# Kernel tuning notes

Hardware: AMD Instinct MI355X
Metric: run time of the kernel (lower is better)

The kernel has to match this reference:

```python
import jax, jax.numpy as jnp
import numpy as np

NUM_HEAD = 8
D_K = 64


def setup_inputs() -> dict:
    key = jax.random.key(0)
    k1, k2, k3 = jax.random.split(key, 3)
    B, S, D = 8, 1024, 512
    input_x = jax.random.normal(k1, (B, S, D), dtype=jnp.float32)
    W_qkv = jax.random.normal(k2, (D, 3 * D), dtype=jnp.float32) * 0.02
    W_out = jax.random.normal(k3, (D, D), dtype=jnp.float32) * 0.02
    return {"input_x": input_x, "W_qkv": W_qkv, "W_out": W_out}


def reference(input_x, W_qkv, W_out):
    B, S, D = input_x.shape
    H, dk = NUM_HEAD, D_K
    qkv = input_x @ W_qkv  # (B, S, 3*D)
    # Faithful to the source: per-head slices OVERLAP.
    # head h: Q=qkv[h*dk:(h+1)*dk], K=qkv[(h+1)*dk:(h+2)*dk], V=qkv[(h+2)*dk:(h+3)*dk]
    Q = qkv[:, :, 0:H * dk].reshape(B, S, H, dk)
    K = qkv[:, :, dk:dk + H * dk].reshape(B, S, H, dk)
    V = qkv[:, :, 2 * dk:2 * dk + H * dk].reshape(B, S, H, dk)
    scale = jnp.asarray(1.0 / np.sqrt(dk), dtype=qkv.dtype)
    scores = jnp.einsum('bqhd,bkhd->bhqk', Q, K) * scale  # (B, H, S, S)
    # nn.Softmax() with dim=None on a 3D (B,S,S) tensor -> legacy dim=0 (batch axis)
    attn = jax.nn.softmax(scores, axis=0)
    out = jnp.einsum('bhqk,bkhd->bqhd', attn, V).reshape(B, S, H * dk)
    return out @ W_out
```

## Files before the change

kernel.cpp:

```cpp
#include <hip/hip_runtime.h>

typedef __bf16 bf16x8 __attribute__((ext_vector_type(8)));
typedef float  f32x4  __attribute__((ext_vector_type(4)));
typedef unsigned short u16x8 __attribute__((ext_vector_type(8)));
typedef unsigned short USHORT;
typedef unsigned int   u32;

__device__ __forceinline__ USHORT f2bf(float f) {
    unsigned u = __float_as_uint(f);
    u += 0x7fffu + ((u >> 16) & 1u);
    return (USHORT)(u >> 16);
}

__device__ __forceinline__ float bf2f(USHORT v) {
    return __uint_as_float((unsigned)v << 16);
}

__device__ __forceinline__ u32 packbf(float lo, float hi) {
    return (u32)f2bf(lo) | ((u32)f2bf(hi) << 16);
}

__device__ __forceinline__ f32x4 fz4() { f32x4 z = {0.f, 0.f, 0.f, 0.f}; return z; }

__device__ __forceinline__ bf16x8 ldbf8(const USHORT* p) { return *(const bf16x8*)p; }

__device__ __forceinline__ f32x4 mfma16(bf16x8 a, bf16x8 b, f32x4 c) {
    return __builtin_amdgcn_mfma_f32_16x16x32_bf16(a, b, c, 0, 0, 0);
}

__device__ __forceinline__ void gload_lds16(const void* g, void* s) {
    __builtin_amdgcn_global_load_lds(
        (const __attribute__((address_space(1))) unsigned int*)g,
        (__attribute__((address_space(3))) unsigned int*)s, 16, 0, 0);
}

__device__ __forceinline__ void lds_fence() {
    asm volatile("s_waitcnt lgkmcnt(0)" ::: "memory");
    __builtin_amdgcn_sched_barrier(0);
}

__global__ __launch_bounds__(256) void prep_kernel(const float* __restrict__ X,
                                                   const float* __restrict__ Wqkv,
                                                   const float* __restrict__ Wout,
                                                   USHORT* __restrict__ Xb,
                                                   USHORT* __restrict__ Wt1,
                                                   USHORT* __restrict__ Wt3) {
    int bid = blockIdx.x;
    if (bid < 2048) {
        int base = (bid * 256 + threadIdx.x) * 8;
        float4 a = *(const float4*)(X + base);
        float4 b = *(const float4*)(X + base + 4);
        u16x8 o;
        o[0] = f2bf(a.x); o[1] = f2bf(a.y); o[2] = f2bf(a.z); o[3] = f2bf(a.w);
        o[4] = f2bf(b.x); o[5] = f2bf(b.y); o[6] = f2bf(b.z); o[7] = f2bf(b.w);
        *(u16x8*)(Xb + base) = o;
    } else if (bid < 3328) {
        int t = (bid - 2048) * 256 + threadIdx.x;
        int k = t & 511, n = t >> 9;
        Wt1[t] = f2bf(Wqkv[(size_t)k * 1536 + n]);
    } else {
        int t = (bid - 3328) * 256 + threadIdx.x;
        int k = t & 511, n = t >> 9;
        Wt3[t] = f2bf(Wout[(size_t)k * 512 + n]);
    }
}

__global__ __launch_bounds__(256) void reduce2(const USHORT* __restrict__ a,
                                               const USHORT* __restrict__ b,
                                               USHORT* __restrict__ o) {
    int base = (blockIdx.x * 256 + threadIdx.x) * 8;
    u16x8 va = *(const u16x8*)(a + base);
    u16x8 vb = *(const u16x8*)(b + base);
    u16x8 out;
#pragma unroll
    for (int j = 0; j < 8; ++j)
        out[j] = f2bf(bf2f(va[j]) + bf2f(vb[j]));
    *(u16x8*)(o + base) = out;
}

template <bool BF16OUT>
__global__ __launch_bounds__(256) void gemm_bt(const USHORT* __restrict__ A,
                                               const USHORT* __restrict__ Bt,
                                               void* __restrict__ Cv,
                                               int M, int N, int K) {
    __shared__ __align__(16) USHORT Asm[128 * 32];
    __shared__ __align__(16) USHORT Bsm[128 * 32];
    const int tid = threadIdx.x;
    const int wv = tid >> 6, ln = tid & 63;
    const int l16 = ln & 15, quad = ln >> 4;
    const int m0 = blockIdx.x * 128, n0 = blockIdx.y * 128;
    const int wm = (wv >> 1) * 64, wn = (wv & 1) * 64;

    f32x4 acc[4][4];
#pragma unroll
    for (int i = 0; i < 4; ++i)
#pragma unroll
        for (int j = 0; j < 4; ++j) acc[i][j] = fz4();

    const int kTiles = K >> 5;
    for (int kt = 0; kt < kTiles; ++kt) {
        __syncthreads();
#pragma unroll
        for (int i = 0; i < 2; ++i) {
            int cb = wv * 128 + i * 64;
            int c = cb + ln;
            gload_lds16(A + (size_t)(m0 + (c >> 2)) * K + kt * 32 + (c & 3) * 8,
                        &Asm[cb * 8]);
            gload_lds16(Bt + (size_t)(n0 + (c >> 2)) * K + kt * 32 + (c & 3) * 8,
                        &Bsm[cb * 8]);
        }
        __syncthreads();

        bf16x8 af[4], bfr[4];
#pragma unroll
        for (int i = 0; i < 4; ++i)
            af[i] = ldbf8(&Asm[(wm + i * 16 + l16) * 32 + quad * 8]);
#pragma unroll
        for (int j = 0; j < 4; ++j)
            bfr[j] = ldbf8(&Bsm[(wn + j * 16 + l16) * 32 + quad * 8]);
#pragma unroll
        for (int i = 0; i < 4; ++i)
#pragma unroll
            for (int j = 0; j < 4; ++j)
                acc[i][j] = mfma16(af[i], bfr[j], acc[i][j]);
    }

#pragma unroll
    for (int i = 0; i < 4; ++i)
#pragma unroll
        for (int j = 0; j < 4; ++j)
#pragma unroll
            for (int r = 0; r < 4; ++r) {
                size_t row = m0 + wm + i * 16 + quad * 4 + r;
                size_t col = n0 + wn + j * 16 + l16;
                if (BF16OUT)
                    ((USHORT*)Cv)[row * N + col] = f2bf(acc[i][j][r]);
                else
                    ((float*)Cv)[row * N + col] = acc[i][j][r];
            }
}

__global__ __launch_bounds__(256) void transpose_v(const USHORT* __restrict__ P,
                                                   USHORT* __restrict__ Vt) {
    __shared__ __align__(16) USHORT T[64][72];
    const int t = threadIdx.x;
    const int k0 = blockIdx.x * 64;
    const int hh = blockIdx.y;
    const int b = blockIdx.z;
#pragma unroll
    for (int i = 0; i < 2; ++i) {
        int c = i * 256 + t;
        int kk = c >> 3, d8 = (c & 7) * 8;
        u16x8 v = *(const u16x8*)(P + (size_t)((b << 10) + k0 + kk) * 640 +
                                  (hh + 2) * 64 + d8);
        *(u16x8*)&T[kk][d8] = v;
    }
    __syncthreads();
#pragma unroll
    for (int i = 0; i < 2; ++i) {
        int d = (t >> 3) + i * 32;
        int kk0 = (t & 7) * 8;
        u16x8 v;
#pragma unroll
        for (int j = 0; j < 8; ++j) v[j] = T[kk0 + j][d];
        *(u16x8*)(Vt + (size_t)(((b << 3) + hh) * 64 + d) * 1024 + k0 + kk0) = v;
    }
}

__global__ __launch_bounds__(256, 1) void attn_kernel(const USHORT* __restrict__ P,
                                                      const USHORT* __restrict__ Vt,
                                                      USHORT* __restrict__ pt0,
                                                      USHORT* __restrict__ pt1) {
    const int bid = blockIdx.x;
    const int g = bid & 15;
    const int h = g >> 1;
    const int kc = g & 1;
    const int qb = bid >> 4;
    const int tid = threadIdx.x;
    const int wv = tid >> 6;
    const int lane = tid & 63;
    const int l16 = lane & 15, quad = lane >> 4;
    const int q0 = qb * 64 + wv * 16;

    __shared__ __align__(16) USHORT Kl[2][16384];
    __shared__ __align__(16) USHORT Vl[2][16384];

    const int qhalf = quad >> 1;
    const bool qodd = (quad & 1) != 0;
    const bool qhi  = quad >= 2;
    const int idx01 = ((qodd ? (2 + qhalf) : qhalf) * 16 + l16) * 4;
    const int idx23 = ((qodd ? qhalf : (2 + qhalf)) * 16 + l16) * 4;

    bf16x8 qf[8][2];
#pragma unroll
    for (int b = 0; b < 8; ++b)
#pragma unroll
        for (int ks = 0; ks < 2; ++ks)
            qf[b][ks] = ldbf8(P + (size_t)((b << 10) + q0 + l16) * 640 + h * 64 +
                              ks * 32 + quad * 8);

    f32x4 oacc[8][4];
#pragma unroll
    for (int b = 0; b < 8; ++b)
#pragma unroll
        for (int nt = 0; nt < 4; ++nt) oacc[b][nt] = fz4();

    auto stage = [&](int k0s, int buf) {
        if (wv < 2) {
#pragma unroll
            for (int i = 0; i < 16; ++i) {
                int gg = wv * 16 + i;
                int b = gg >> 2, ks = (gg >> 1) & 1, half = gg & 1;
                gload_lds16(P + (size_t)((b << 10) + k0s + half * 16 + (lane & 15)) * 640 +
                                (h + 1) * 64 + ks * 32 + (lane >> 4) * 8,
                            &Kl[buf][(b * 2 + ks) * 1024 + half * 512]);
            }
        } else {
#pragma unroll
            for (int i = 0; i < 16; ++i) {
                int gg = (wv - 2) * 16 + i;
                int b = gg >> 2, dq = gg & 3;
                gload_lds16(Vt + (size_t)(((b << 3) + h) * 64 + dq * 16 + (lane & 15)) * 1024 +
                                k0s + (lane >> 4) * 8,
                            &Vl[buf][b * 2048 + dq * 512]);
            }
        }
    };

    const int kbase = kc * 512;
    stage(kbase, 0);
    __syncthreads();

    int buf = 0;
    for (int it = 0; it < 16; ++it) {
        if (it < 15) stage(kbase + (it + 1) * 32, buf ^ 1);

        const USHORT* Kb = Kl[buf];
        const USHORT* Vb = Vl[buf];

        f32x4 sacc[8][2];
#pragma unroll
        for (int b = 0; b < 8; ++b) { sacc[b][0] = fz4(); sacc[b][1] = fz4(); }
#pragma unroll
        for (int ks = 0; ks < 2; ++ks)
#pragma unroll
            for (int nt = 0; nt < 2; ++nt) {
                bf16x8 kf[8];
#pragma unroll
                for (int b = 0; b < 8; ++b)
                    kf[b] = ldbf8(&Kb[(b * 2 + ks) * 1024 + nt * 512 + lane * 8]);
#pragma unroll
                for (int b = 0; b < 8; ++b)
                    sacc[b][nt] = mfma16(kf[b], qf[b][ks], sacc[b][nt]);
            }

#pragma unroll
        for (int nt = 0; nt < 2; ++nt)
#pragma unroll
            for (int r = 0; r < 4; ++r) {
                float e[8];
                float Z = 0.f;
#pragma unroll
                for (int b = 0; b < 8; ++b) {
                    e[b] = __builtin_amdgcn_exp2f(sacc[b][nt][r] * 0.1803368801f);
                    Z += e[b];
                }
                float inv = __builtin_amdgcn_rcpf(Z);
#pragma unroll
                for (int b = 0; b < 8; ++b)
                    sacc[b][nt][r] = e[b] * inv;
            }

#pragma unroll
        for (int b = 0; b < 8; ++b) {
            u32 w00 = packbf(sacc[b][0][0], sacc[b][0][1]);
            u32 w01 = packbf(sacc[b][0][2], sacc[b][0][3]);
            u32 w10 = packbf(sacc[b][1][0], sacc[b][1][1]);
            u32 w11 = packbf(sacc[b][1][2], sacc[b][1][3]);
            u32 s0 = qodd ? w10 : w00, s1 = qodd ? w11 : w01;
            u32 s2 = qodd ? w00 : w10, s3 = qodd ? w01 : w11;
            u32 r0 = (u32)__builtin_amdgcn_ds_permute(idx01, (int)s0);
            u32 r1 = (u32)__builtin_amdgcn_ds_permute(idx01, (int)s1);
            u32 r2 = (u32)__builtin_amdgcn_ds_permute(idx23, (int)s2);
            u32 r3 = (u32)__builtin_amdgcn_ds_permute(idx23, (int)s3);
            union { u32 u[4]; bf16x8 v; } pu;
            pu.u[0] = qhi ? r2 : r0;
            pu.u[1] = qhi ? r3 : r1;
            pu.u[2] = qhi ? r0 : r2;
            pu.u[3] = qhi ? r1 : r3;
            bf16x8 pb = pu.v;

            bf16x8 vf[4];
#pragma unroll
            for (int nt = 0; nt < 4; ++nt)
                vf[nt] = ldbf8(&Vb[b * 2048 + nt * 512 + lane * 8]);
#pragma unroll
            for (int nt = 0; nt < 4; ++nt)
                oacc[b][nt] = mfma16(vf[nt], pb, oacc[b][nt]);
        }

        __syncthreads();
        buf ^= 1;
    }

    USHORT* part = kc ? pt1 : pt0;
    USHORT* ep = ((USHORT*)Kl) + wv * (16 * 72);
#pragma unroll
    for (int b = 0; b < 8; ++b) {
#pragma unroll
        for (int nt = 0; nt < 4; ++nt)
#pragma unroll
            for (int r = 0; r < 4; ++r)
                ep[l16 * 72 + nt * 16 + quad * 4 + r] = f2bf(oacc[b][nt][r]);
        lds_fence();
#pragma unroll
        for (int half = 0; half < 2; ++half) {
            int row = half * 8 + (lane >> 3);
            int seg = lane & 7;
            u16x8 v = *(const u16x8*)&ep[row * 72 + seg * 8];
            *(u16x8*)(part + (size_t)((b << 10) + q0 + row) * 512 + h * 64 + seg * 8) = v;
        }
        lds_fence();
    }
}

extern "C" void kernel_launch(void* const* d_in, const int* in_sizes, int n_in,
                              void* d_out, int out_size, void* d_ws, size_t ws_size,
                              hipStream_t stream) {
    const float* X = (const float*)d_in[0];
    const float* Wqkv = (const float*)d_in[1];
    const float* Wout = (const float*)d_in[2];
    float* out = (float*)d_out;

    char* w = (char*)d_ws;
    USHORT* Xb  = (USHORT*)(w);
    USHORT* Wt1 = (USHORT*)(w + 8388608);
    USHORT* Wt3 = (USHORT*)(w + 9043968);
    USHORT* P   = (USHORT*)(w + 9568256);
    USHORT* Vt  = (USHORT*)(w + 20054016);
    USHORT* pt1 = (USHORT*)(w + 28442624);
    USHORT* pt0 = Xb;
    USHORT* CtxB = Xb;

    prep_kernel<<<4352, 256, 0, stream>>>(X, Wqkv, Wout, Xb, Wt1, Wt3);
    gemm_bt<true><<<dim3(64, 5), 256, 0, stream>>>(Xb, Wt1, (void*)P, 8192, 640, 512);
    transpose_v<<<dim3(16, 8, 8), 256, 0, stream>>>(P, Vt);
    attn_kernel<<<256, 256, 0, stream>>>(P, Vt, pt0, pt1);
    reduce2<<<2048, 256, 0, stream>>>(pt0, pt1, CtxB);
    gemm_bt<false><<<dim3(64, 4), 256, 0, stream>>>(CtxB, Wt3, (void*)out, 8192, 512, 512);
}
```

Measured before the change: 175.7 us.

## Split attention keys four ways, single-buffer LDS, two blocks per CU

The attention kernel now splits the key dimension into four chunks instead of two, doubling the grid to 512 blocks. LDS double buffering is dropped to halve shared memory, and launch bounds allow two blocks per CU. The goal is more occupancy and fewer idle CUs on a 256-CU part. The cost is extra partial-output traffic in a four-way reduction and loss of load/compute overlap inside each block.

```diff
diff --git a/kernel.cpp b/kernel.cpp
--- a/kernel.cpp
+++ b/kernel.cpp
@@ -65,16 +65,20 @@
     }
 }
 
-__global__ __launch_bounds__(256) void reduce2(const USHORT* __restrict__ a,
+__global__ __launch_bounds__(256) void reduce4(const USHORT* __restrict__ a,
                                                const USHORT* __restrict__ b,
+                                               const USHORT* __restrict__ c,
+                                               const USHORT* __restrict__ d,
                                                USHORT* __restrict__ o) {
     int base = (blockIdx.x * 256 + threadIdx.x) * 8;
     u16x8 va = *(const u16x8*)(a + base);
     u16x8 vb = *(const u16x8*)(b + base);
+    u16x8 vc = *(const u16x8*)(c + base);
+    u16x8 vd = *(const u16x8*)(d + base);
     u16x8 out;
 #pragma unroll
     for (int j = 0; j < 8; ++j)
-        out[j] = f2bf(bf2f(va[j]) + bf2f(vb[j]));
+        out[j] = f2bf(bf2f(va[j]) + bf2f(vb[j]) + bf2f(vc[j]) + bf2f(vd[j]));
     *(u16x8*)(o + base) = out;
 }
 
@@ -167,23 +171,25 @@
     }
 }
 
-__global__ __launch_bounds__(256, 1) void attn_kernel(const USHORT* __restrict__ P,
+__global__ __launch_bounds__(256, 2) void attn_kernel(const USHORT* __restrict__ P,
                                                       const USHORT* __restrict__ Vt,
                                                       USHORT* __restrict__ pt0,
-                                                      USHORT* __restrict__ pt1) {
+                                                      USHORT* __restrict__ pt1,
+                                                      USHORT* __restrict__ pt2,
+                                                      USHORT* __restrict__ pt3) {
     const int bid = blockIdx.x;
-    const int g = bid & 15;
-    const int h = g >> 1;
-    const int kc = g & 1;
-    const int qb = bid >> 4;
+    const int g = bid & 31;
+    const int h = g >> 2;
+    const int kc = g & 3;
+    const int qb = bid >> 5;
     const int tid = threadIdx.x;
     const int wv = tid >> 6;
     const int lane = tid & 63;
     const int l16 = lane & 15, quad = lane >> 4;
     const int q0 = qb * 64 + wv * 16;
 
-    __shared__ __align__(16) USHORT Kl[2][16384];
-    __shared__ __align__(16) USHORT Vl[2][16384];
+    __shared__ __align__(16) USHORT Kl[16384];
+    __shared__ __align__(16) USHORT Vl[16384];
 
     const int qhalf = quad >> 1;
     const bool qodd = (quad & 1) != 0;
@@ -205,15 +211,19 @@
 #pragma unroll
         for (int nt = 0; nt < 4; ++nt) oacc[b][nt] = fz4();
 
-    auto stage = [&](int k0s, int buf) {
+    const int kbase = kc * 256;
+    for (int it = 0; it < 8; ++it) {
+        const int k0 = kbase + it * 32;
+
+        __syncthreads();
         if (wv < 2) {
 #pragma unroll
             for (int i = 0; i < 16; ++i) {
                 int gg = wv * 16 + i;
                 int b = gg >> 2, ks = (gg >> 1) & 1, half = gg & 1;
-                gload_lds16(P + (size_t)((b << 10) + k0s + half * 16 + (lane & 15)) * 640 +
+                gload_lds16(P + (size_t)((b << 10) + k0 + half * 16 + (lane & 15)) * 640 +
                                 (h + 1) * 64 + ks * 32 + (lane >> 4) * 8,
-                            &Kl[buf][(b * 2 + ks) * 1024 + half * 512]);
+                            &Kl[(b * 2 + ks) * 1024 + half * 512]);
             }
         } else {
 #pragma unroll
@@ -221,22 +231,11 @@
                 int gg = (wv - 2) * 16 + i;
                 int b = gg >> 2, dq = gg & 3;
                 gload_lds16(Vt + (size_t)(((b << 3) + h) * 64 + dq * 16 + (lane & 15)) * 1024 +
-                                k0s + (lane >> 4) * 8,
-                            &Vl[buf][b * 2048 + dq * 512]);
+                                k0 + (lane >> 4) * 8,
+                            &Vl[b * 2048 + dq * 512]);
             }
         }
-    };
-
-    const int kbase = kc * 512;
-    stage(kbase, 0);
-    __syncthreads();
-
-    int buf = 0;
-    for (int it = 0; it < 16; ++it) {
-        if (it < 15) stage(kbase + (it + 1) * 32, buf ^ 1);
-
-        const USHORT* Kb = Kl[buf];
-        const USHORT* Vb = Vl[buf];
+        __syncthreads();
 
         f32x4 sacc[8][2];
 #pragma unroll
@@ -248,7 +247,7 @@
                 bf16x8 kf[8];
 #pragma unroll
                 for (int b = 0; b < 8; ++b)
-                    kf[b] = ldbf8(&Kb[(b * 2 + ks) * 1024 + nt * 512 + lane * 8]);
+                    kf[b] = ldbf8(&Kl[(b * 2 + ks) * 1024 + nt * 512 + lane * 8]);
 #pragma unroll
                 for (int b = 0; b < 8; ++b)
                     sacc[b][nt] = mfma16(kf[b], qf[b][ks], sacc[b][nt]);
@@ -293,17 +292,15 @@
             bf16x8 vf[4];
 #pragma unroll
             for (int nt = 0; nt < 4; ++nt)
-                vf[nt] = ldbf8(&Vb[b * 2048 + nt * 512 + lane * 8]);
+                vf[nt] = ldbf8(&Vl[b * 2048 + nt * 512 + lane * 8]);
 #pragma unroll
             for (int nt = 0; nt < 4; ++nt)
                 oacc[b][nt] = mfma16(vf[nt], pb, oacc[b][nt]);
         }
-
-        __syncthreads();
-        buf ^= 1;
-    }
-
-    USHORT* part = kc ? pt1 : pt0;
+    }
+
+    __syncthreads();
+    USHORT* part = (kc == 0) ? pt0 : (kc == 1) ? pt1 : (kc == 2) ? pt2 : pt3;
     USHORT* ep = ((USHORT*)Kl) + wv * (16 * 72);
 #pragma unroll
     for (int b = 0; b < 8; ++b) {
@@ -339,13 +336,15 @@
     USHORT* P   = (USHORT*)(w + 9568256);
     USHORT* Vt  = (USHORT*)(w + 20054016);
     USHORT* pt1 = (USHORT*)(w + 28442624);
+    USHORT* pt2 = (USHORT*)(w + 36831232);
+    USHORT* pt3 = (USHORT*)(w + 45219840);
     USHORT* pt0 = Xb;
     USHORT* CtxB = Xb;
 
     prep_kernel<<<4352, 256, 0, stream>>>(X, Wqkv, Wout, Xb, Wt1, Wt3);
     gemm_bt<true><<<dim3(64, 5), 256, 0, stream>>>(Xb, Wt1, (void*)P, 8192, 640, 512);
     transpose_v<<<dim3(16, 8, 8), 256, 0, stream>>>(P, Vt);
-    attn_kernel<<<256, 256, 0, stream>>>(P, Vt, pt0, pt1);
-    reduce2<<<2048, 256, 0, stream>>>(pt0, pt1, CtxB);
+    attn_kernel<<<512, 256, 0, stream>>>(P, Vt, pt0, pt1, pt2, pt3);
+    reduce4<<<2048, 256, 0, stream>>>(pt0, pt1, pt2, pt3, CtxB);
     gemm_bt<false><<<dim3(64, 4), 256, 0, stream>>>(CtxB, Wt3, (void*)out, 8192, 512, 512);
 }
```

After: 262.2 us. 49.2% more time.

## Split batch across wave pairs in attention, doubling blocks and dropping double buffering

Applied to the files above, without the earlier changes.

The attention kernel now splits the 8-batch softmax axis across pairs of waves, and each pair covers 16 query rows, so each block handles 32 queries and the grid grows from 256 to 512 blocks. The two halves of the softmax denominator are exchanged through a small shared-memory array with an extra barrier per iteration. K/V staging drops its double buffer, which halves LDS use and, together with launch_bounds(256,2), allows two blocks per CU, at the cost of losing overlap between loads and compute. Packing to bf16 now uses the hardware v_cvt_pk_bf16_f32 instruction instead of manual rounding. K/V tiles are now loaded twice as often overall, since each block covers fewer queries.

```diff
diff --git a/kernel.cpp b/kernel.cpp
--- a/kernel.cpp
+++ b/kernel.cpp
@@ -16,8 +16,10 @@
     return __uint_as_float((unsigned)v << 16);
 }
 
-__device__ __forceinline__ u32 packbf(float lo, float hi) {
-    return (u32)f2bf(lo) | ((u32)f2bf(hi) << 16);
+__device__ __forceinline__ u32 cvtpk(float lo, float hi) {
+    u32 r;
+    asm("v_cvt_pk_bf16_f32 %0, %1, %2" : "=v"(r) : "v"(lo), "v"(hi));
+    return r;
 }
 
 __device__ __forceinline__ f32x4 fz4() { f32x4 z = {0.f, 0.f, 0.f, 0.f}; return z; }
@@ -167,7 +169,7 @@
     }
 }
 
-__global__ __launch_bounds__(256, 1) void attn_kernel(const USHORT* __restrict__ P,
+__global__ __launch_bounds__(256, 2) void attn_kernel(const USHORT* __restrict__ P,
                                                       const USHORT* __restrict__ Vt,
                                                       USHORT* __restrict__ pt0,
                                                       USHORT* __restrict__ pt1) {
@@ -178,12 +180,15 @@
     const int qb = bid >> 4;
     const int tid = threadIdx.x;
     const int wv = tid >> 6;
+    const int qt = wv >> 1;
+    const int bhalf = wv & 1;
     const int lane = tid & 63;
     const int l16 = lane & 15, quad = lane >> 4;
-    const int q0 = qb * 64 + wv * 16;
-
-    __shared__ __align__(16) USHORT Kl[2][16384];
-    __shared__ __align__(16) USHORT Vl[2][16384];
+    const int q0 = qb * 32 + qt * 16;
+
+    __shared__ __align__(16) USHORT Kl[16384];
+    __shared__ __align__(16) USHORT Vl[16384];
+    __shared__ __align__(16) float  zex[4][64][8];
 
     const int qhalf = quad >> 1;
     const bool qodd = (quad & 1) != 0;
@@ -191,29 +196,33 @@
     const int idx01 = ((qodd ? (2 + qhalf) : qhalf) * 16 + l16) * 4;
     const int idx23 = ((qodd ? qhalf : (2 + qhalf)) * 16 + l16) * 4;
 
-    bf16x8 qf[8][2];
-#pragma unroll
-    for (int b = 0; b < 8; ++b)
+    bf16x8 qf[4][2];
+#pragma unroll
+    for (int b = 0; b < 4; ++b)
 #pragma unroll
         for (int ks = 0; ks < 2; ++ks)
-            qf[b][ks] = ldbf8(P + (size_t)((b << 10) + q0 + l16) * 640 + h * 64 +
-                              ks * 32 + quad * 8);
-
-    f32x4 oacc[8][4];
-#pragma unroll
-    for (int b = 0; b < 8; ++b)
+            qf[b][ks] = ldbf8(P + (size_t)(((bhalf * 4 + b) << 10) + q0 + l16) * 640 +
+                              h * 64 + ks * 32 + quad * 8);
+
+    f32x4 oacc[4][4];
+#pragma unroll
+    for (int b = 0; b < 4; ++b)
 #pragma unroll
         for (int nt = 0; nt < 4; ++nt) oacc[b][nt] = fz4();
 
-    auto stage = [&](int k0s, int buf) {
+    const int kbase = kc * 512;
+    for (int it = 0; it < 16; ++it) {
+        const int k0 = kbase + it * 32;
+
+        __syncthreads();
         if (wv < 2) {
 #pragma unroll
             for (int i = 0; i < 16; ++i) {
                 int gg = wv * 16 + i;
                 int b = gg >> 2, ks = (gg >> 1) & 1, half = gg & 1;
-                gload_lds16(P + (size_t)((b << 10) + k0s + half * 16 + (lane & 15)) * 640 +
+                gload_lds16(P + (size_t)((b << 10) + k0 + half * 16 + (lane & 15)) * 640 +
                                 (h + 1) * 64 + ks * 32 + (lane >> 4) * 8,
-                            &Kl[buf][(b * 2 + ks) * 1024 + half * 512]);
+                            &Kl[(b * 2 + ks) * 1024 + half * 512]);
             }
         } else {
 #pragma unroll
@@ -221,62 +230,63 @@
                 int gg = (wv - 2) * 16 + i;
                 int b = gg >> 2, dq = gg & 3;
                 gload_lds16(Vt + (size_t)(((b << 3) + h) * 64 + dq * 16 + (lane & 15)) * 1024 +
-                                k0s + (lane >> 4) * 8,
-                            &Vl[buf][b * 2048 + dq * 512]);
+                                k0 + (lane >> 4) * 8,
+                            &Vl[b * 2048 + dq * 512]);
             }
         }
-    };
-
-    const int kbase = kc * 512;
-    stage(kbase, 0);
-    __syncthreads();
-
-    int buf = 0;
-    for (int it = 0; it < 16; ++it) {
-        if (it < 15) stage(kbase + (it + 1) * 32, buf ^ 1);
-
-        const USHORT* Kb = Kl[buf];
-        const USHORT* Vb = Vl[buf];
-
-        f32x4 sacc[8][2];
-#pragma unroll
-        for (int b = 0; b < 8; ++b) { sacc[b][0] = fz4(); sacc[b][1] = fz4(); }
+        __syncthreads();
+
+        f32x4 sacc[4][2];
+#pragma unroll
+        for (int b = 0; b < 4; ++b) { sacc[b][0] = fz4(); sacc[b][1] = fz4(); }
 #pragma unroll
         for (int ks = 0; ks < 2; ++ks)
 #pragma unroll
             for (int nt = 0; nt < 2; ++nt) {
-                bf16x8 kf[8];
-#pragma unroll
-                for (int b = 0; b < 8; ++b)
-                    kf[b] = ldbf8(&Kb[(b * 2 + ks) * 1024 + nt * 512 + lane * 8]);
-#pragma unroll
-                for (int b = 0; b < 8; ++b)
+                bf16x8 kf[4];
+#pragma unroll
+                for (int b = 0; b < 4; ++b)
+                    kf[b] = ldbf8(&Kl[((bhalf * 4 + b) * 2 + ks) * 1024 + nt * 512 + lane * 8]);
+#pragma unroll
+                for (int b = 0; b < 4; ++b)
                     sacc[b][nt] = mfma16(kf[b], qf[b][ks], sacc[b][nt]);
             }
 
+        f32x4 zh[2];
 #pragma unroll
         for (int nt = 0; nt < 2; ++nt)
 #pragma unroll
             for (int r = 0; r < 4; ++r) {
-                float e[8];
-                float Z = 0.f;
-#pragma unroll
-                for (int b = 0; b < 8; ++b) {
-                    e[b] = __builtin_amdgcn_exp2f(sacc[b][nt][r] * 0.1803368801f);
-                    Z += e[b];
+                float z = 0.f;
+#pragma unroll
+                for (int b = 0; b < 4; ++b) {
+                    float e = __builtin_amdgcn_exp2f(sacc[b][nt][r] * 0.1803368801f);
+                    sacc[b][nt][r] = e;
+                    z += e;
                 }
-                float inv = __builtin_amdgcn_rcpf(Z);
-#pragma unroll
-                for (int b = 0; b < 8; ++b)
-                    sacc[b][nt][r] = e[b] * inv;
-            }
-
-#pragma unroll
-        for (int b = 0; b < 8; ++b) {
-            u32 w00 = packbf(sacc[b][0][0], sacc[b][0][1]);
-            u32 w01 = packbf(sacc[b][0][2], sacc[b][0][3]);
-            u32 w10 = packbf(sacc[b][1][0], sacc[b][1][1]);
-            u32 w11 = packbf(sacc[b][1][2], sacc[b][1][3]);
+                zh[nt][r] = z;
+            }
+        *(f32x4*)&zex[wv][lane][0] = zh[0];
+        *(f32x4*)&zex[wv][lane][4] = zh[1];
+        __syncthreads();
+        f32x4 zp0 = *(const f32x4*)&zex[wv ^ 1][lane][0];
+        f32x4 zp1 = *(const f32x4*)&zex[wv ^ 1][lane][4];
+#pragma unroll
+        for (int nt = 0; nt < 2; ++nt)
+#pragma unroll
+            for (int r = 0; r < 4; ++r) {
+                float inv = __builtin_amdgcn_rcpf(zh[nt][r] + (nt ? zp1[r] : zp0[r]));
+#pragma unroll
+                for (int b = 0; b < 4; ++b)
+                    sacc[b][nt][r] *= inv;
+            }
+
+#pragma unroll
+        for (int b = 0; b < 4; ++b) {
+            u32 w00 = cvtpk(sacc[b][0][0], sacc[b][0][1]);
+            u32 w01 = cvtpk(sacc[b][0][2], sacc[b][0][3]);
+            u32 w10 = cvtpk(sacc[b][1][0], sacc[b][1][1]);
+            u32 w11 = cvtpk(sacc[b][1][2], sacc[b][1][3]);
             u32 s0 = qodd ? w10 : w00, s1 = qodd ? w11 : w01;
             u32 s2 = qodd ? w00 : w10, s3 = qodd ? w01 : w11;
             u32 r0 = (u32)__builtin_amdgcn_ds_permute(idx01, (int)s0);
@@ -293,20 +303,19 @@
             bf16x8 vf[4];
 #pragma unroll
             for (int nt = 0; nt < 4; ++nt)
-                vf[nt] = ldbf8(&Vb[b * 2048 + nt * 512 + lane * 8]);
+                vf[nt] = ldbf8(&Vl[(bhalf * 4 + b) * 2048 + nt * 512 + lane * 8]);
 #pragma unroll
             for (int nt = 0; nt < 4; ++nt)
                 oacc[b][nt] = mfma16(vf[nt], pb, oacc[b][nt]);
         }
-
-        __syncthreads();
-        buf ^= 1;
-    }
-
+    }
+
+    __syncthreads();
     USHORT* part = kc ? pt1 : pt0;
     USHORT* ep = ((USHORT*)Kl) + wv * (16 * 72);
 #pragma unroll
-    for (int b = 0; b < 8; ++b) {
+    for (int b = 0; b < 4; ++b) {
+        const int bs = bhalf * 4 + b;
 #pragma unroll
         for (int nt = 0; nt < 4; ++nt)
 #pragma unroll
@@ -318,7 +327,7 @@
             int row = half * 8 + (lane >> 3);
             int seg = lane & 7;
             u16x8 v = *(const u16x8*)&ep[row * 72 + seg * 8];
-            *(u16x8*)(part + (size_t)((b << 10) + q0 + row) * 512 + h * 64 + seg * 8) = v;
+            *(u16x8*)(part + (size_t)((bs << 10) + q0 + row) * 512 + h * 64 + seg * 8) = v;
         }
         lds_fence();
     }
@@ -345,7 +354,7 @@
     prep_kernel<<<4352, 256, 0, stream>>>(X, Wqkv, Wout, Xb, Wt1, Wt3);
     gemm_bt<true><<<dim3(64, 5), 256, 0, stream>>>(Xb, Wt1, (void*)P, 8192, 640, 512);
     transpose_v<<<dim3(16, 8, 8), 256, 0, stream>>>(P, Vt);
-    attn_kernel<<<256, 256, 0, stream>>>(P, Vt, pt0, pt1);
+    attn_kernel<<<512, 256, 0, stream>>>(P, Vt, pt0, pt1);
     reduce2<<<2048, 256, 0, stream>>>(pt0, pt1, CtxB);
     gemm_bt<false><<<dim3(64, 4), 256, 0, stream>>>(CtxB, Wt3, (void*)out, 8192, 512, 512);
 }
```

Measured after the change: 180.3 us. +2.6%, slower.

## Fuse partial-sum reduction into output GEMM and halve GEMM N-tile

Applied to the files above, without the earlier changes.

Removes the separate reduce2 kernel by summing the two bf16 attention partials while loading the A tile in the output projection GEMM. Both GEMMs now use a 128x64 tile, which doubles the number of blocks (64x10 and 64x8 grids) to fill more CUs. It also swaps manual float-to-bf16 rounding for the hardware v_cvt_pk_bf16_f32 packed conversion. The fused path loads A through registers instead of async global-to-LDS, which may stall the inner loop, and the smaller tile loses some reuse.

```diff
diff --git a/kernel.cpp b/kernel.cpp
--- a/kernel.cpp
+++ b/kernel.cpp
@@ -16,8 +16,10 @@
     return __uint_as_float((unsigned)v << 16);
 }
 
-__device__ __forceinline__ u32 packbf(float lo, float hi) {
-    return (u32)f2bf(lo) | ((u32)f2bf(hi) << 16);
+__device__ __forceinline__ u32 cvtpk(float lo, float hi) {
+    u32 r;
+    asm("v_cvt_pk_bf16_f32 %0, %1, %2" : "=v"(r) : "v"(lo), "v"(hi));
+    return r;
 }
 
 __device__ __forceinline__ f32x4 fz4() { f32x4 z = {0.f, 0.f, 0.f, 0.f}; return z; }
@@ -65,37 +67,25 @@
     }
 }
 
-__global__ __launch_bounds__(256) void reduce2(const USHORT* __restrict__ a,
-                                               const USHORT* __restrict__ b,
-                                               USHORT* __restrict__ o) {
-    int base = (blockIdx.x * 256 + threadIdx.x) * 8;
-    u16x8 va = *(const u16x8*)(a + base);
-    u16x8 vb = *(const u16x8*)(b + base);
-    u16x8 out;
-#pragma unroll
-    for (int j = 0; j < 8; ++j)
-        out[j] = f2bf(bf2f(va[j]) + bf2f(vb[j]));
-    *(u16x8*)(o + base) = out;
-}
-
-template <bool BF16OUT>
-__global__ __launch_bounds__(256) void gemm_bt(const USHORT* __restrict__ A,
-                                               const USHORT* __restrict__ Bt,
-                                               void* __restrict__ Cv,
-                                               int M, int N, int K) {
+template <bool BF16OUT, bool SUM2>
+__global__ __launch_bounds__(256, 2) void gemm_bn64(const USHORT* __restrict__ A0,
+                                                    const USHORT* __restrict__ A1,
+                                                    const USHORT* __restrict__ Bt,
+                                                    void* __restrict__ Cv,
+                                                    int M, int N, int K) {
     __shared__ __align__(16) USHORT Asm[128 * 32];
-    __shared__ __align__(16) USHORT Bsm[128 * 32];
+    __shared__ __align__(16) USHORT Bsm[64 * 32];
     const int tid = threadIdx.x;
     const int wv = tid >> 6, ln = tid & 63;
     const int l16 = ln & 15, quad = ln >> 4;
-    const int m0 = blockIdx.x * 128, n0 = blockIdx.y * 128;
-    const int wm = (wv >> 1) * 64, wn = (wv & 1) * 64;
-
-    f32x4 acc[4][4];
+    const int m0 = blockIdx.x * 128, n0 = blockIdx.y * 64;
+    const int wm = (wv >> 1) * 64, wn = (wv & 1) * 32;
+
+    f32x4 acc[4][2];
 #pragma unroll
     for (int i = 0; i < 4; ++i)
 #pragma unroll
-        for (int j = 0; j < 4; ++j) acc[i][j] = fz4();
+        for (int j = 0; j < 2; ++j) acc[i][j] = fz4();
 
     const int kTiles = K >> 5;
     for (int kt = 0; kt < kTiles; ++kt) {
@@ -104,31 +94,46 @@
         for (int i = 0; i < 2; ++i) {
             int cb = wv * 128 + i * 64;
             int c = cb + ln;
-            gload_lds16(A + (size_t)(m0 + (c >> 2)) * K + kt * 32 + (c & 3) * 8,
-                        &Asm[cb * 8]);
+            size_t aoff = (size_t)(m0 + (c >> 2)) * K + kt * 32 + (c & 3) * 8;
+            if (SUM2) {
+                u16x8 a0 = *(const u16x8*)(A0 + aoff);
+                u16x8 a1 = *(const u16x8*)(A1 + aoff);
+                union { u32 u[4]; u16x8 v; } s;
+#pragma unroll
+                for (int j = 0; j < 4; ++j)
+                    s.u[j] = cvtpk(bf2f(a0[2 * j]) + bf2f(a1[2 * j]),
+                                   bf2f(a0[2 * j + 1]) + bf2f(a1[2 * j + 1]));
+                *(u16x8*)&Asm[c * 8] = s.v;
+            } else {
+                gload_lds16(A0 + aoff, &Asm[cb * 8]);
+            }
+        }
+        {
+            int cb = wv * 64;
+            int c = cb + ln;
             gload_lds16(Bt + (size_t)(n0 + (c >> 2)) * K + kt * 32 + (c & 3) * 8,
                         &Bsm[cb * 8]);
         }
         __syncthreads();
 
-        bf16x8 af[4], bfr[4];
+        bf16x8 af[4], bfr[2];
 #pragma unroll
         for (int i = 0; i < 4; ++i)
             af[i] = ldbf8(&Asm[(wm + i * 16 + l16) * 32 + quad * 8]);
 #pragma unroll
-        for (int j = 0; j < 4; ++j)
+        for (int j = 0; j < 2; ++j)
             bfr[j] = ldbf8(&Bsm[(wn + j * 16 + l16) * 32 + quad * 8]);
 #pragma unroll
         for (int i = 0; i < 4; ++i)
 #pragma unroll
-            for (int j = 0; j < 4; ++j)
+            for (int j = 0; j < 2; ++j)
                 acc[i][j] = mfma16(af[i], bfr[j], acc[i][j]);
     }
 
 #pragma unroll
     for (int i = 0; i < 4; ++i)
 #pragma unroll
-        for (int j = 0; j < 4; ++j)
+        for (int j = 0; j < 2; ++j)
 #pragma unroll
             for (int r = 0; r < 4; ++r) {
                 size_t row = m0 + wm + i * 16 + quad * 4 + r;
@@ -273,10 +278,10 @@
 
 #pragma unroll
         for (int b = 0; b < 8; ++b) {
-            u32 w00 = packbf(sacc[b][0][0], sacc[b][0][1]);
-            u32 w01 = packbf(sacc[b][0][2], sacc[b][0][3]);
-            u32 w10 = packbf(sacc[b][1][0], sacc[b][1][1]);
-            u32 w11 = packbf(sacc[b][1][2], sacc[b][1][3]);
+            u32 w00 = cvtpk(sacc[b][0][0], sacc[b][0][1]);
+            u32 w01 = cvtpk(sacc[b][0][2], sacc[b][0][3]);
+            u32 w10 = cvtpk(sacc[b][1][0], sacc[b][1][1]);
+            u32 w11 = cvtpk(sacc[b][1][2], sacc[b][1][3]);
             u32 s0 = qodd ? w10 : w00, s1 = qodd ? w11 : w01;
             u32 s2 = qodd ? w00 : w10, s3 = qodd ? w01 : w11;
             u32 r0 = (u32)__builtin_amdgcn_ds_permute(idx01, (int)s0);
@@ -340,12 +345,12 @@
     USHORT* Vt  = (USHORT*)(w + 20054016);
     USHORT* pt1 = (USHORT*)(w + 28442624);
     USHORT* pt0 = Xb;
-    USHORT* CtxB = Xb;
 
     prep_kernel<<<4352, 256, 0, stream>>>(X, Wqkv, Wout, Xb, Wt1, Wt3);
-    gemm_bt<true><<<dim3(64, 5), 256, 0, stream>>>(Xb, Wt1, (void*)P, 8192, 640, 512);
+    gemm_bn64<true, false><<<dim3(64, 10), 256, 0, stream>>>(Xb, nullptr, Wt1,
+                                                             (void*)P, 8192, 640, 512);
     transpose_v<<<dim3(16, 8, 8), 256, 0, stream>>>(P, Vt);
     attn_kernel<<<256, 256, 0, stream>>>(P, Vt, pt0, pt1);
-    reduce2<<<2048, 256, 0, stream>>>(pt0, pt1, CtxB);
-    gemm_bt<false><<<dim3(64, 4), 256, 0, stream>>>(CtxB, Wt3, (void*)out, 8192, 512, 512);
-}
+    gemm_bn64<false, true><<<dim3(64, 8), 256, 0, stream>>>(pt0, pt1, Wt3,
+                                                            (void*)out, 8192, 512, 512);
+}
```

Result: faster. 169.3 us (-3.7%).
